# Kernel tuning notes

Measured on AMD Instinct MI355X. Metric: run time of the kernel, lower is better.

Reference implementation:

```python
import jax, jax.numpy as jnp
import numpy as np

KSIZE = 20      # gaussian smoothing kernel size
SIGMA = 2.0     # gaussianSmoothWidth
STRIDE = 4      # strideLen
KLEN = 14       # kernelLen
LN_EPS = 1e-5


def _gauss_smooth(x):
    # x: [B, T, D]; depthwise conv1d along time, padding='same' (torch: left 9, right 10)
    D = x.shape[-1]
    i = jnp.arange(KSIZE, dtype=x.dtype)
    g = jnp.exp(-0.5 * ((i - (KSIZE - 1) / 2.0) / SIGMA) ** 2)
    g = g / jnp.sum(g)
    k = jnp.tile(g[None, None, :], (D, 1, 1))  # [D, 1, KSIZE]
    y = jax.lax.conv_general_dilated(
        jnp.swapaxes(x, 1, 2), k,
        window_strides=(1,), padding=[(9, 10)],
        feature_group_count=D,
        dimension_numbers=('NCW', 'OIW', 'NCW'))
    return jnp.swapaxes(y, 1, 2)


def _qrnn_layer(x, W, b):
    # SpeechBrain QuasiRNNLayer (output_gate=True, unidirectional, zoneout=0)
    # x: [B, T, F]; W: [3H, 2F]; b: [3H]
    xprev = jnp.concatenate([jnp.zeros_like(x[:, :1]), x[:, :-1]], axis=1)
    y = jnp.einsum('btf,gf->btg', jnp.concatenate([x, xprev], axis=-1), W) + b
    z, f, o = jnp.split(y, 3, axis=-1)
    z = jnp.tanh(z)
    f = jax.nn.sigmoid(f)
    fz = f * z
    # recurrence: c_t = f_t*z_t + (1-f_t)*c_{t-1}, c_0-input = 0
    def step(c, ins):
        f_t, fz_t = ins
        c = fz_t + (1.0 - f_t) * c
        return c, c
    c0 = jnp.zeros((f.shape[0], f.shape[2]), f.dtype)
    _, cs = jax.lax.scan(step, c0, (jnp.swapaxes(f, 0, 1), jnp.swapaxes(fz, 0, 1)))
    c = jnp.swapaxes(cs, 0, 1)  # [B, T, H]
    return jax.nn.sigmoid(o) * c


def reference(neuralInput, dayWeights, dayBias, w0, b0, w_rest, b_rest,
              ln_gamma, ln_beta, w_out, b_out, dayIdx):
    x = _gauss_smooth(neuralInput)                    # [B, T, D]
    Wd = dayWeights[dayIdx]                           # [B, D, D]
    bd = dayBias[dayIdx]                              # [B, 1, D]
    x = jnp.einsum('btd,bdk->btk', x, Wd) + bd
    x = x / (1.0 + jnp.abs(x))                        # Softsign
    B, T, D = x.shape
    Tp = (T - KLEN) // STRIDE + 1
    idx = jnp.arange(Tp)[:, None] * STRIDE + jnp.arange(KLEN)[None, :]
    win = x[:, idx, :]                                # [B, Tp, K, D]
    # torch Unfold ordering: channel-major -> feature index = d*KLEN + k
    strided = jnp.transpose(win, (0, 1, 3, 2)).reshape(B, Tp, D * KLEN)
    h = _qrnn_layer(strided, w0, b0)
    for i in range(w_rest.shape[0]):
        h = _qrnn_layer(h, w_rest[i], b_rest[i])
    mu = jnp.mean(h, axis=-1, keepdims=True)
    var = jnp.mean(jnp.square(h - mu), axis=-1, keepdims=True)
    hn = (h - mu) * jax.lax.rsqrt(var + LN_EPS) * ln_gamma + ln_beta
    return jnp.einsum('bth,ch->btc', hn, w_out) + b_out


def setup_inputs() -> dict:
    key = jax.random.key(0)
    ks = jax.random.split(key, 10)
    B, T, D, H, L, NDAYS, C = 32, 2000, 256, 512, 3, 24, 41
    F0 = D * KLEN  # 3584
    inp = {}
    inp['neuralInput'] = jax.random.normal(ks[0], (B, T, D), jnp.float32)
    inp['dayIdx'] = jax.random.randint(ks[1], (B,), 0, NDAYS, jnp.int64 if jax.config.jax_enable_x64 else jnp.int32)
    eye = jnp.eye(D, dtype=jnp.float32)
    inp['dayWeights'] = eye[None] + 0.02 * jax.random.normal(ks[2], (NDAYS, D, D), jnp.float32)
    inp['dayBias'] = jnp.zeros((NDAYS, 1, D), jnp.float32)
    inp['w0'] = jax.random.normal(ks[3], (3 * H, 2 * F0), jnp.float32) / np.sqrt(2 * F0)
    inp['b0'] = jnp.zeros((3 * H,), jnp.float32)
    inp['w_rest'] = jax.random.normal(ks[4], (L - 1, 3 * H, 2 * H), jnp.float32) / np.sqrt(2 * H)
    inp['b_rest'] = jnp.zeros((L - 1, 3 * H), jnp.float32)
    inp['ln_gamma'] = jnp.ones((H,), jnp.float32)
    inp['ln_beta'] = jnp.zeros((H,), jnp.float32)
    inp['w_out'] = jax.random.normal(ks[5], (C, H), jnp.float32) / np.sqrt(H)
    inp['b_out'] = jnp.zeros((C,), jnp.float32)
    return inp
```

## Files before the change

### kernel.cpp

```cpp
#include <hip/hip_runtime.h>
#include <hip/hip_bf16.h>

typedef __hip_bfloat16 bf16;
typedef __attribute__((ext_vector_type(8))) short bf16x8;
typedef __attribute__((ext_vector_type(4))) float f32x4;

#define GT 16
__global__ __launch_bounds__(256) void gauss_kernel(const float* __restrict__ X,
                                                    bf16* __restrict__ Y, int T) {
  int b = blockIdx.y, t0 = blockIdx.x * GT;
  int tid = threadIdx.x;
  __shared__ float xs[GT + 19][256];
  const float* xb = X + (long)b * T * 256;
  for (int r = 0; r < GT + 19; ++r) {
    int tt = t0 + r - 9;
    xs[r][tid] = (tt >= 0 && tt < T) ? xb[(long)tt * 256 + tid] : 0.f;
  }
  __syncthreads();
  float g[20];
  float norm = 0.f;
#pragma unroll
  for (int j = 0; j < 20; ++j) {
    float u = (j - 9.5f) * 0.5f;
    g[j] = expf(-0.5f * u * u);
    norm += g[j];
  }
  float rn = 1.f / norm;
  for (int i = 0; i < GT; ++i) {
    int t = t0 + i;
    if (t >= T) break;
    float acc = 0.f;
#pragma unroll
    for (int j = 0; j < 20; ++j) acc += g[j] * xs[i + j][tid];
    Y[((long)b * T + t) * 256 + tid] = (bf16)(acc * rn);
  }
}

__global__ __launch_bounds__(256) void transpose_day(const float* __restrict__ W,
                                                     bf16* __restrict__ Wt) {
  __shared__ float tile[64][65];
  int d0 = blockIdx.x * 64, g0 = blockIdx.y * 64, day = blockIdx.z;
  const float* Wd = W + (long)day * 65536;
  int tx = threadIdx.x & 63, ty = threadIdx.x >> 6;
  for (int i = 0; i < 16; ++i) {
    int d = ty + i * 4;
    tile[d][tx] = Wd[(long)(d0 + d) * 256 + g0 + tx];
  }
  __syncthreads();
  bf16* out = Wt + (long)day * 65536;
  for (int i = 0; i < 16; ++i) {
    int g = ty + i * 4;
    out[(long)(g0 + g) * 256 + d0 + tx] = (bf16)tile[tx][g];
  }
}

__global__ void buildV_kernel(const float* __restrict__ w0, bf16* __restrict__ V) {
  long idx = (long)blockIdx.x * 256 + threadIdx.x;
  const long total = 18L * 1536 * 256;
  if (idx >= total) return;
  int u = (int)(idx / (1536 * 256));
  int r = (int)(idx % (1536 * 256));
  int g = r >> 8, d = r & 255;
  float v = 0.f;
  if (u < 14) v += w0[(long)g * 7168 + 3584 + d * 14 + u];
  if (u >= 4) v += w0[(long)g * 7168 + d * 14 + (u - 4)];
  V[idx] = (bf16)v;
}

__global__ void conv_wrest(const float* __restrict__ in, bf16* __restrict__ out, long n) {
  long i = (long)blockIdx.x * 256 + threadIdx.x;
  if (i >= n) return;
  long g = i >> 10;
  int k = (int)(i & 1023);
  out[i] = (bf16)in[(g << 10) | (long)(k ^ 512)];
}

__global__ void conv_w0half(const float* __restrict__ in, bf16* __restrict__ out) {
  long i = (long)blockIdx.x * 256 + threadIdx.x;
  const long n = 1536L * 3584;
  if (i >= n) return;
  long g = i / 3584;
  int j = (int)(i - g * 3584);
  out[i] = (bf16)in[g * 7168 + j];
}

__global__ void zero_pads(bf16* __restrict__ h1s, bf16* __restrict__ h2s) {
  int i = blockIdx.x * 256 + threadIdx.x;
  if (i >= 16384) return;
  int b = i >> 9, k = i & 511;
  h1s[(long)b * 498 * 512 + k] = (bf16)0.f;
  h2s[(long)b * 498 * 512 + k] = (bf16)0.f;
}

__global__ __launch_bounds__(256) void mfma_gemm(
    const bf16* __restrict__ A, const bf16* __restrict__ W,
    const float* __restrict__ bias, float* __restrict__ Yf,
    bf16* __restrict__ Yb, const int* __restrict__ dayIdx,
    long astride, int Ta, int D, int rstride, int Tm, int N, int tstride,
    int ntaps, int tap_off0, long wsg, long wst, long dayWStride,
    int dayBStride, int epilogue) {
  int b = blockIdx.z;
  int t0 = blockIdx.y * 128, g0 = blockIdx.x * 128;
  const bf16* Ab = A + (long)b * astride;
  long wbase = 0;
  int boff = 0;
  if (dayIdx) {
    int di = dayIdx[b];
    wbase = (long)di * dayWStride;
    boff = di * dayBStride;
  }
  __shared__ __align__(16) bf16 Al[2][128 * 64];
  __shared__ __align__(16) bf16 Wl[2][128 * 64];
  int tid = threadIdx.x;
  int lane = tid & 63;
  int wave = tid >> 6;
  int wm = (wave >> 1) * 64, wn = (wave & 1) * 64;
  int lr = lane & 15, lg = lane >> 4;
  int srow = tid >> 3, su = tid & 7;
  int nch = D >> 6;
  int niter = ntaps * nch;
  f32x4 acc[4][4] = {};
  bf16x8 ra[4], rw[4];

  auto issue = [&](int it) {
    int tap = it / nch;
    int d0 = (it - tap * nch) << 6;
    int off = tap + tap_off0;
    const bf16* Wtap = W + wbase + (long)tap * wst;
#pragma unroll
    for (int i = 0; i < 4; ++i) {
      int m = srow + i * 32;
      int t = t0 + m;
      int time = t * tstride + off;
      bf16x8 v = {};
      if (t < Tm && time >= 0 && time < Ta)
        v = *reinterpret_cast<const bf16x8*>(Ab + (long)time * rstride + d0 + su * 8);
      ra[i] = v;
      rw[i] = *reinterpret_cast<const bf16x8*>(Wtap + (long)(g0 + m) * wsg + d0 + su * 8);
    }
  };
  auto write_lds = [&](int bufi) {
#pragma unroll
    for (int i = 0; i < 4; ++i) {
      int m = srow + i * 32;
      *reinterpret_cast<bf16x8*>(&Al[bufi][m * 64 + ((su ^ (m & 7)) << 3)]) = ra[i];
      *reinterpret_cast<bf16x8*>(&Wl[bufi][m * 64 + ((su ^ (m & 7)) << 3)]) = rw[i];
    }
  };

  issue(0);
  write_lds(0);
  __syncthreads();
  int cur = 0;
  for (int it = 0; it < niter; ++it) {
    if (it + 1 < niter) issue(it + 1);
#pragma unroll
    for (int kc = 0; kc < 2; ++kc) {
      int ub = kc * 4 + lg;
      bf16x8 af[4], bw[4];
#pragma unroll
      for (int f = 0; f < 4; ++f) {
        int m = wm + f * 16 + lr;
        af[f] = *reinterpret_cast<const bf16x8*>(&Al[cur][m * 64 + ((ub ^ (m & 7)) << 3)]);
        int g = wn + f * 16 + lr;
        bw[f] = *reinterpret_cast<const bf16x8*>(&Wl[cur][g * 64 + ((ub ^ (g & 7)) << 3)]);
      }
      __builtin_amdgcn_s_setprio(1);
#pragma unroll
      for (int fm = 0; fm < 4; ++fm)
#pragma unroll
        for (int fn = 0; fn < 4; ++fn)
          acc[fm][fn] = __builtin_amdgcn_mfma_f32_16x16x32_bf16(af[fm], bw[fn],
                                                                acc[fm][fn], 0, 0, 0);
      __builtin_amdgcn_s_setprio(0);
    }
    if (it + 1 < niter) write_lds(cur ^ 1);
    __syncthreads();
    cur ^= 1;
  }
#pragma unroll
  for (int fn = 0; fn < 4; ++fn) {
    int gcol = g0 + wn + fn * 16 + lr;
    float bb = bias[boff + gcol];
#pragma unroll
    for (int fm = 0; fm < 4; ++fm) {
#pragma unroll
      for (int r = 0; r < 4; ++r) {
        int t = t0 + wm + fm * 16 + lg * 4 + r;
        if (t >= Tm) continue;
        float v = acc[fm][fn][r] + bb;
        if (epilogue == 1) {
          v = v / (1.f + fabsf(v));
          Yb[((long)b * Tm + t) * N + gcol] = (bf16)v;
        } else {
          Yf[((long)b * Tm + t) * N + gcol] = v;
        }
      }
    }
  }
}

__global__ void build_A0(const bf16* __restrict__ xs, bf16* __restrict__ A0) {
  int idx = blockIdx.x * 256 + threadIdx.x;
  if (idx >= 32 * 3584) return;
  int b = idx / 3584, j = idx % 3584;
  int d = j / 14, u = j % 14;
  A0[idx] = xs[((long)b * 2000 + u) * 256 + d];
}

__global__ __launch_bounds__(256) void t0_gemm(const bf16* __restrict__ A0,
                                               const bf16* __restrict__ W0b,
                                               float* __restrict__ part) {
  int g0 = blockIdx.x * 128;
  int ks = blockIdx.y;
  int k0 = ks * 512;
  __shared__ __align__(16) bf16 Wl[128 * 64];
  __shared__ __align__(16) bf16 Alds[32 * 64];
  int tid = threadIdx.x;
  int lane = tid & 63, wave = tid >> 6;
  int wn = wave * 32;
  int lr = lane & 15, lg = lane >> 4;
  int srow = tid >> 3, su = tid & 7;
  f32x4 acc[2][2] = {};
  for (int c = 0; c < 8; ++c) {
    int d0 = k0 + c * 64;
#pragma unroll
    for (int i = 0; i < 4; ++i) {
      int m = srow + i * 32;
      *reinterpret_cast<bf16x8*>(&Wl[m * 64 + ((su ^ (m & 7)) << 3)]) =
          *reinterpret_cast<const bf16x8*>(W0b + (long)(g0 + m) * 3584 + d0 + su * 8);
    }
    {
      int m = srow;
      *reinterpret_cast<bf16x8*>(&Alds[m * 64 + ((su ^ (m & 7)) << 3)]) =
          *reinterpret_cast<const bf16x8*>(A0 + (long)m * 3584 + d0 + su * 8);
    }
    __syncthreads();
#pragma unroll
    for (int kc = 0; kc < 2; ++kc) {
      int ub = kc * 4 + lg;
      bf16x8 am[2], bw[2];
#pragma unroll
      for (int f = 0; f < 2; ++f) {
        int m = f * 16 + lr;
        am[f] = *reinterpret_cast<const bf16x8*>(&Alds[m * 64 + ((ub ^ (m & 7)) << 3)]);
        int g = wn + f * 16 + lr;
        bw[f] = *reinterpret_cast<const bf16x8*>(&Wl[g * 64 + ((ub ^ (g & 7)) << 3)]);
      }
#pragma unroll
      for (int fm = 0; fm < 2; ++fm)
#pragma unroll
        for (int fn = 0; fn < 2; ++fn)
          acc[fm][fn] = __builtin_amdgcn_mfma_f32_16x16x32_bf16(am[fm], bw[fn],
                                                                acc[fm][fn], 0, 0, 0);
    }
    __syncthreads();
  }
#pragma unroll
  for (int fn = 0; fn < 2; ++fn) {
    int gcol = g0 + wn + fn * 16 + lr;
#pragma unroll
    for (int fm = 0; fm < 2; ++fm)
#pragma unroll
      for (int r = 0; r < 4; ++r) {
        int brow = fm * 16 + lg * 4 + r;
        part[((long)ks * 32 + brow) * 1536 + gcol] = acc[fm][fn][r];
      }
  }
}

__global__ void t0_reduce(const float* __restrict__ part, const float* __restrict__ b0,
                          float* __restrict__ y, int Tp) {
  int idx = blockIdx.x * 256 + threadIdx.x;
  if (idx >= 32 * 1536) return;
  int b = idx / 1536, g = idx % 1536;
  float s = b0[g];
#pragma unroll
  for (int k = 0; k < 7; ++k) s += part[((long)k * 32 + b) * 1536 + g];
  y[(long)b * Tp * 1536 + g] = s;
}

#define NC 8
#define LC 63
__device__ __forceinline__ float fsig(float x) { return 1.f / (1.f + __expf(-x)); }
__device__ __forceinline__ float ftanh(float x) { return 1.f - 2.f / (1.f + __expf(2.f * x)); }

__global__ __launch_bounds__(256) void scan_pass1(const float* __restrict__ Yv,
                                                  float* __restrict__ Afac,
                                                  float* __restrict__ Bfac, int Tp) {
  int idx = blockIdx.x * 256 + threadIdx.x;
  int ci = idx >> 14;
  int chain = idx & 16383;
  int b = chain >> 9, hh = chain & 511;
  const float* yb = Yv + (long)b * Tp * 1536 + hh;
  int t0 = ci * LC, t1 = min(t0 + LC, Tp);
  float A = 1.f, Bv = 0.f;
  for (int t = t0; t < t1; ++t) {
    const float* p = yb + (long)t * 1536;
    float z = p[0], f = p[512];
    float fs = fsig(f);
    Bv = fs * ftanh(z) + (1.f - fs) * Bv;
    A *= (1.f - fs);
  }
  Afac[idx] = A;
  Bfac[idx] = Bv;
}

__global__ void scan_pass2(const float* __restrict__ Afac, const float* __restrict__ Bfac,
                           float* __restrict__ cst) {
  int chain = blockIdx.x * 256 + threadIdx.x;
  float c = 0.f;
#pragma unroll
  for (int ci = 0; ci < NC; ++ci) {
    cst[ci * 16384 + chain] = c;
    c = Afac[ci * 16384 + chain] * c + Bfac[ci * 16384 + chain];
  }
}

__global__ __launch_bounds__(256) void scan_pass3(const float* __restrict__ Yv,
                                                  const float* __restrict__ cst,
                                                  bf16* __restrict__ H, int Tp) {
  int idx = blockIdx.x * 256 + threadIdx.x;
  int ci = idx >> 14;
  int chain = idx & 16383;
  int b = chain >> 9, hh = chain & 511;
  const float* yb = Yv + (long)b * Tp * 1536 + hh;
  bf16* hb = H + ((long)b * 498 + 1) * 512 + hh;
  int t0 = ci * LC, t1 = min(t0 + LC, Tp);
  float c = cst[ci * 16384 + chain];
  for (int t = t0; t < t1; ++t) {
    const float* p = yb + (long)t * 1536;
    float z = p[0], f = p[512], o = p[1024];
    float fs = fsig(f);
    c = fs * ftanh(z) + (1.f - fs) * c;
    hb[(long)t * 512] = (bf16)(fsig(o) * c);
  }
}

__global__ __launch_bounds__(256) void ln_out_kernel(
    const bf16* __restrict__ Hs, const float* __restrict__ gamma,
    const float* __restrict__ beta, const float* __restrict__ Wo,
    const float* __restrict__ bo, float* __restrict__ Out) {
  long bt = blockIdx.x;
  int b = (int)(bt / 497), t = (int)(bt % 497);
  const bf16* hrow = Hs + ((long)b * 498 + 1 + t) * 512;
  int tid = threadIdx.x;
  float v0 = (float)hrow[tid], v1 = (float)hrow[tid + 256];
  float s = v0 + v1, s2 = v0 * v0 + v1 * v1;
#pragma unroll
  for (int d = 32; d; d >>= 1) {
    s += __shfl_down(s, d);
    s2 += __shfl_down(s2, d);
  }
  __shared__ float rs[4], rs2[4];
  int wid = tid >> 6, lane = tid & 63;
  if (lane == 0) {
    rs[wid] = s;
    rs2[wid] = s2;
  }
  __syncthreads();
  float sum = rs[0] + rs[1] + rs[2] + rs[3];
  float sum2 = rs2[0] + rs2[1] + rs2[2] + rs2[3];
  float mu = sum * (1.f / 512.f);
  float var = sum2 * (1.f / 512.f) - mu * mu;
  float rstd = rsqrtf(var + 1e-5f);
  __shared__ float hl[512];
  hl[tid] = (v0 - mu) * rstd * gamma[tid] + beta[tid];
  hl[tid + 256] = (v1 - mu) * rstd * gamma[tid + 256] + beta[tid + 256];
  __syncthreads();
  const float4* hp = reinterpret_cast<const float4*>(&hl[lane * 8]);
  float4 h0v = hp[0], h1v = hp[1];
  for (int c = wid; c < 41; c += 4) {
    const float4* wp = reinterpret_cast<const float4*>(Wo + (long)c * 512 + lane * 8);
    float4 w0v = wp[0], w1v = wp[1];
    float a = w0v.x * h0v.x + w0v.y * h0v.y + w0v.z * h0v.z + w0v.w * h0v.w +
              w1v.x * h1v.x + w1v.y * h1v.y + w1v.z * h1v.z + w1v.w * h1v.w;
#pragma unroll
    for (int d = 32; d; d >>= 1) a += __shfl_down(a, d);
    if (lane == 0) Out[bt * 41 + c] = a + bo[c];
  }
}

extern "C" void kernel_launch(void* const* d_in, const int* in_sizes, int n_in,
                              void* d_out, int out_size, void* d_ws, size_t ws_size,
                              hipStream_t stream) {
  const float* neuralInput = (const float*)d_in[0];
  const int* dayIdx = (const int*)d_in[1];
  const float* dayWeights = (const float*)d_in[2];
  const float* dayBias = (const float*)d_in[3];
  const float* w0 = (const float*)d_in[4];
  const float* b0 = (const float*)d_in[5];
  const float* w_rest = (const float*)d_in[6];
  const float* b_rest = (const float*)d_in[7];
  const float* ln_gamma = (const float*)d_in[8];
  const float* ln_beta = (const float*)d_in[9];
  const float* w_out = (const float*)d_in[10];
  const float* b_out = (const float*)d_in[11];
  float* out = (float*)d_out;

  const int B = 32, T = 2000, Tp = 497;

  char* p = (char*)d_ws;
  float* y = (float*)p;   p += 97714176;
  bf16* xs0b = (bf16*)p;  p += 32768000;
  bf16* xs = (bf16*)p;    p += 32768000;
  bf16* Vb = (bf16*)p;    p += 14155776;
  bf16* dWb = (bf16*)p;   p += 3145728;
  bf16* wrb = (bf16*)p;   p += 6291456;
  bf16* w0b = (bf16*)p;   p += 11010048;
  bf16* A0 = (bf16*)p;    p += 229376;
  float* part = (float*)p; p += 1376256;
  bf16* h1s = (bf16*)p;   p += 16320512;
  bf16* h2s = (bf16*)p;   p += 16320512;
  float* Afac = (float*)p; p += 524288;
  float* Bfac = (float*)p; p += 524288;
  float* cst = (float*)p;  p += 524288;

  hipLaunchKernelGGL(zero_pads, dim3(64), dim3(256), 0, stream, h1s, h2s);
  hipLaunchKernelGGL(gauss_kernel, dim3((T + GT - 1) / GT, B), dim3(256), 0, stream,
                     neuralInput, xs0b, T);
  hipLaunchKernelGGL(transpose_day, dim3(4, 4, 24), dim3(256), 0, stream, dayWeights, dWb);
  hipLaunchKernelGGL(buildV_kernel, dim3((18L * 1536 * 256 + 255) / 256), dim3(256), 0,
                     stream, w0, Vb);
  hipLaunchKernelGGL(conv_wrest, dim3((2L * 1536 * 1024 + 255) / 256), dim3(256), 0,
                     stream, w_rest, wrb, 2L * 1536 * 1024);
  hipLaunchKernelGGL(conv_w0half, dim3((1536L * 3584 + 255) / 256), dim3(256), 0,
                     stream, w0, w0b);
  hipLaunchKernelGGL(mfma_gemm, dim3(2, 16, B), dim3(256), 0, stream, xs0b, dWb,
                     dayBias, (float*)nullptr, xs, dayIdx, (long)T * 256, T, 256, 256,
                     T, 256, 1, 1, 0, 256L, 0L, 65536L, 256, 1);
  hipLaunchKernelGGL(build_A0, dim3((32 * 3584 + 255) / 256), dim3(256), 0, stream, xs, A0);
  hipLaunchKernelGGL(t0_gemm, dim3(12, 7), dim3(256), 0, stream, A0, w0b, part);
  hipLaunchKernelGGL(mfma_gemm, dim3(12, 4, B), dim3(256), 0, stream, xs, Vb, b0, y,
                     (bf16*)nullptr, (const int*)nullptr, (long)T * 256, T, 256, 256,
                     Tp, 1536, 4, 18, -4, 256L, 1536L * 256, 0L, 0, 0);
  hipLaunchKernelGGL(t0_reduce, dim3((32 * 1536 + 255) / 256), dim3(256), 0, stream,
                     part, b0, y, Tp);
  hipLaunchKernelGGL(scan_pass1, dim3(512), dim3(256), 0, stream, y, Afac, Bfac, Tp);
  hipLaunchKernelGGL(scan_pass2, dim3(64), dim3(256), 0, stream, Afac, Bfac, cst);
  hipLaunchKernelGGL(scan_pass3, dim3(512), dim3(256), 0, stream, y, cst, h1s, Tp);
  for (int i = 0; i < 2; ++i) {
    bf16* hin = (i == 0) ? h1s : h2s;
    bf16* hout = (i == 0) ? h2s : h1s;
    hipLaunchKernelGGL(mfma_gemm, dim3(12, 4, B), dim3(256), 0, stream, hin,
                       wrb + (long)i * 1536 * 1024, b_rest + (long)i * 1536, y,
                       (bf16*)nullptr, (const int*)nullptr, 498L * 512, Tp, 1024, 512,
                       Tp, 1536, 1, 1, 0, 1024L, 0L, 0L, 0, 0);
    hipLaunchKernelGGL(scan_pass1, dim3(512), dim3(256), 0, stream, y, Afac, Bfac, Tp);
    hipLaunchKernelGGL(scan_pass2, dim3(64), dim3(256), 0, stream, Afac, Bfac, cst);
    hipLaunchKernelGGL(scan_pass3, dim3(512), dim3(256), 0, stream, y, cst, hout, Tp);
  }
  hipLaunchKernelGGL(ln_out_kernel, dim3(B * Tp), dim3(256), 0, stream, h1s,
                     ln_gamma, ln_beta, w_out, b_out, out);
}
```

Before: 944.4 us.

## Use direct global-to-LDS loads, blocked weight layouts, bf16 activated gate outputs

Replaces the register-staged double-buffered GEMM with a single-buffered kernel that loads tiles straight into LDS via global_load_lds. Weights are pre-arranged into 64-wide K-blocks so the loads are contiguous, and out-of-range rows read from a zero page. The GEMM epilogue now applies tanh/sigmoid and stores bf16 instead of fp32 pre-activations, halving the traffic the scan kernels read. The weight-prep kernels are merged into one launch. Dropping double buffering may expose load latency.

```diff
diff --git a/kernel.cpp b/kernel.cpp
--- a/kernel.cpp
+++ b/kernel.cpp
@@ -4,6 +4,9 @@
 typedef __hip_bfloat16 bf16;
 typedef __attribute__((ext_vector_type(8))) short bf16x8;
 typedef __attribute__((ext_vector_type(4))) float f32x4;
+
+__device__ __forceinline__ float fsig(float x) { return 1.f / (1.f + __expf(-x)); }
+__device__ __forceinline__ float ftanh(float x) { return 1.f - 2.f / (1.f + __expf(2.f * x)); }
 
 #define GT 16
 __global__ __launch_bounds__(256) void gauss_kernel(const float* __restrict__ X,
@@ -47,154 +50,150 @@
     tile[d][tx] = Wd[(long)(d0 + d) * 256 + g0 + tx];
   }
   __syncthreads();
-  bf16* out = Wt + (long)day * 65536;
+  bf16* outp = Wt + (((long)day * 4 + (d0 >> 6)) * 256 + g0) * 64;
   for (int i = 0; i < 16; ++i) {
     int g = ty + i * 4;
-    out[(long)(g0 + g) * 256 + d0 + tx] = (bf16)tile[tx][g];
-  }
-}
-
-__global__ void buildV_kernel(const float* __restrict__ w0, bf16* __restrict__ V) {
-  long idx = (long)blockIdx.x * 256 + threadIdx.x;
-  const long total = 18L * 1536 * 256;
-  if (idx >= total) return;
-  int u = (int)(idx / (1536 * 256));
-  int r = (int)(idx % (1536 * 256));
-  int g = r >> 8, d = r & 255;
-  float v = 0.f;
-  if (u < 14) v += w0[(long)g * 7168 + 3584 + d * 14 + u];
-  if (u >= 4) v += w0[(long)g * 7168 + d * 14 + (u - 4)];
-  V[idx] = (bf16)v;
-}
-
-__global__ void conv_wrest(const float* __restrict__ in, bf16* __restrict__ out, long n) {
+    outp[(long)g * 64 + tx] = (bf16)tile[tx][g];
+  }
+}
+
+__global__ void prep_misc(const float* __restrict__ w0, const float* __restrict__ w_rest,
+                          bf16* __restrict__ V2, bf16* __restrict__ wrb2,
+                          bf16* __restrict__ w0b, bf16* __restrict__ h1s,
+                          bf16* __restrict__ h2s, bf16* __restrict__ zpage) {
   long i = (long)blockIdx.x * 256 + threadIdx.x;
-  if (i >= n) return;
-  long g = i >> 10;
-  int k = (int)(i & 1023);
-  out[i] = (bf16)in[(g << 10) | (long)(k ^ 512)];
-}
-
-__global__ void conv_w0half(const float* __restrict__ in, bf16* __restrict__ out) {
-  long i = (long)blockIdx.x * 256 + threadIdx.x;
-  const long n = 1536L * 3584;
-  if (i >= n) return;
-  long g = i / 3584;
-  int j = (int)(i - g * 3584);
-  out[i] = (bf16)in[g * 7168 + j];
-}
-
-__global__ void zero_pads(bf16* __restrict__ h1s, bf16* __restrict__ h2s) {
-  int i = blockIdx.x * 256 + threadIdx.x;
-  if (i >= 16384) return;
-  int b = i >> 9, k = i & 511;
-  h1s[(long)b * 498 * 512 + k] = (bf16)0.f;
-  h2s[(long)b * 498 * 512 + k] = (bf16)0.f;
-}
-
-__global__ __launch_bounds__(256) void mfma_gemm(
+  if (i < 7077888L) {
+    int u = (int)(i / (1536 * 256));
+    int r = (int)(i % (1536 * 256));
+    int g = r >> 8, d = r & 255;
+    float v = 0.f;
+    if (u < 14) v += w0[(long)g * 7168 + 3584 + d * 14 + u];
+    if (u >= 4) v += w0[(long)g * 7168 + d * 14 + (u - 4)];
+    V2[(((long)u * 4 + (d >> 6)) * 1536 + g) * 64 + (d & 63)] = (bf16)v;
+    return;
+  }
+  i -= 7077888L;
+  if (i < 3145728L) {
+    int L = (int)(i / (1536 * 1024));
+    int r = (int)(i % (1536 * 1024));
+    int g = r >> 10, k = r & 1023;
+    float v = w_rest[(long)L * 1536 * 1024 + (long)g * 1024 + (k ^ 512)];
+    wrb2[(long)L * 16 * 1536 * 64 + ((long)(k >> 6) * 1536 + g) * 64 + (k & 63)] = (bf16)v;
+    return;
+  }
+  i -= 3145728L;
+  if (i < 5505024L) {
+    long g = i / 3584;
+    int j = (int)(i - g * 3584);
+    w0b[i] = (bf16)w0[g * 7168 + j];
+    return;
+  }
+  i -= 5505024L;
+  if (i < 16384) {
+    int b = (int)(i >> 9), k = (int)(i & 511);
+    h1s[(long)b * 498 * 512 + k] = (bf16)0.f;
+    h2s[(long)b * 498 * 512 + k] = (bf16)0.f;
+    return;
+  }
+  i -= 16384;
+  if (i < 128) zpage[i] = (bf16)0.f;
+}
+
+__global__ __launch_bounds__(256, 4) void mfma97(
     const bf16* __restrict__ A, const bf16* __restrict__ W,
-    const float* __restrict__ bias, float* __restrict__ Yf,
-    bf16* __restrict__ Yb, const int* __restrict__ dayIdx,
-    long astride, int Ta, int D, int rstride, int Tm, int N, int tstride,
-    int ntaps, int tap_off0, long wsg, long wst, long dayWStride,
-    int dayBStride, int epilogue) {
-  int b = blockIdx.z;
-  int t0 = blockIdx.y * 128, g0 = blockIdx.x * 128;
-  const bf16* Ab = A + (long)b * astride;
+    const float* __restrict__ bias, bf16* __restrict__ Y,
+    const int* __restrict__ dayIdx, const bf16* __restrict__ zpage,
+    long astride, int Ta, int rstride, int Tm, int N, int tstride,
+    int ntaps, int nch, int tap_off0, int NW, long dayWStride,
+    int dayBStride, int mode, int nti, int ngi) {
+  __shared__ __align__(16) char smem[32768];
+  const int id = blockIdx.x;
+  const int bi = id / (ngi * nti);
+  const int rem = id - bi * (ngi * nti);
+  const int gi = rem / nti;
+  const int ti = rem - gi * nti;
+  const int g0 = gi * 128, t0 = ti * 128;
+
+  const bf16* Ab = A + (long)bi * astride;
   long wbase = 0;
   int boff = 0;
   if (dayIdx) {
-    int di = dayIdx[b];
+    int di = dayIdx[bi];
     wbase = (long)di * dayWStride;
     boff = di * dayBStride;
   }
-  __shared__ __align__(16) bf16 Al[2][128 * 64];
-  __shared__ __align__(16) bf16 Wl[2][128 * 64];
-  int tid = threadIdx.x;
-  int lane = tid & 63;
-  int wave = tid >> 6;
-  int wm = (wave >> 1) * 64, wn = (wave & 1) * 64;
-  int lr = lane & 15, lg = lane >> 4;
-  int srow = tid >> 3, su = tid & 7;
-  int nch = D >> 6;
-  int niter = ntaps * nch;
+  const int tid = threadIdx.x;
+  const int lane = tid & 63;
+  const int w = tid >> 6;
+  const int wm = (w >> 1) * 64, wn = (w & 1) * 64;
+  const int lr = lane & 15, lg = lane >> 4;
+
   f32x4 acc[4][4] = {};
-  bf16x8 ra[4], rw[4];
-
-  auto issue = [&](int it) {
-    int tap = it / nch;
-    int d0 = (it - tap * nch) << 6;
-    int off = tap + tap_off0;
-    const bf16* Wtap = W + wbase + (long)tap * wst;
-#pragma unroll
-    for (int i = 0; i < 4; ++i) {
-      int m = srow + i * 32;
-      int t = t0 + m;
-      int time = t * tstride + off;
-      bf16x8 v = {};
-      if (t < Tm && time >= 0 && time < Ta)
-        v = *reinterpret_cast<const bf16x8*>(Ab + (long)time * rstride + d0 + su * 8);
-      ra[i] = v;
-      rw[i] = *reinterpret_cast<const bf16x8*>(Wtap + (long)(g0 + m) * wsg + d0 + su * 8);
+
+  for (int tap = 0; tap < ntaps; ++tap) {
+    for (int dblk = 0; dblk < nch; ++dblk) {
+      int d0 = dblk << 6;
+      int s = tap * nch + dblk;
+      const bf16* Wp = W + wbase + ((long)s * NW + g0) * 64;
+#pragma unroll
+      for (int j = 0; j < 8; ++j) {
+        int q = j * 256 + tid;
+        int qw = j * 256 + w * 64;
+        const bf16* src;
+        if (j < 4) {
+          int row = q >> 3;
+          int u = (q & 7) ^ (row & 7);
+          int time = (t0 + row) * tstride + tap + tap_off0;
+          src = (time >= 0 && time < Ta) ? Ab + (long)time * rstride + d0 + u * 8
+                                         : zpage;
+        } else {
+          int row = (q >> 3) - 128;
+          int u = (q & 7) ^ (row & 7);
+          src = Wp + row * 64 + u * 8;
+        }
+        auto lp = (__attribute__((address_space(3))) void*)(smem + qw * 16);
+        __builtin_amdgcn_global_load_lds(
+            (const __attribute__((address_space(1))) void*)src, lp, 16, 0, 0);
+      }
+      __syncthreads();
+#pragma unroll
+      for (int kc = 0; kc < 2; ++kc) {
+        int ub = kc * 4 + lg;
+        bf16x8 af[4], bw[4];
+#pragma unroll
+        for (int f = 0; f < 4; ++f) {
+          int m = wm + f * 16 + lr;
+          af[f] = *reinterpret_cast<const bf16x8*>(smem + m * 128 + ((ub ^ (m & 7)) << 4));
+          int g = wn + f * 16 + lr;
+          bw[f] = *reinterpret_cast<const bf16x8*>(smem + 16384 + g * 128 +
+                                                   ((ub ^ (g & 7)) << 4));
+        }
+#pragma unroll
+        for (int fm = 0; fm < 4; ++fm)
+#pragma unroll
+          for (int fn = 0; fn < 4; ++fn)
+            acc[fm][fn] = __builtin_amdgcn_mfma_f32_16x16x32_bf16(af[fm], bw[fn],
+                                                                  acc[fm][fn], 0, 0, 0);
+      }
+      __syncthreads();
     }
-  };
-  auto write_lds = [&](int bufi) {
-#pragma unroll
-    for (int i = 0; i < 4; ++i) {
-      int m = srow + i * 32;
-      *reinterpret_cast<bf16x8*>(&Al[bufi][m * 64 + ((su ^ (m & 7)) << 3)]) = ra[i];
-      *reinterpret_cast<bf16x8*>(&Wl[bufi][m * 64 + ((su ^ (m & 7)) << 3)]) = rw[i];
-    }
-  };
-
-  issue(0);
-  write_lds(0);
-  __syncthreads();
-  int cur = 0;
-  for (int it = 0; it < niter; ++it) {
-    if (it + 1 < niter) issue(it + 1);
-#pragma unroll
-    for (int kc = 0; kc < 2; ++kc) {
-      int ub = kc * 4 + lg;
-      bf16x8 af[4], bw[4];
-#pragma unroll
-      for (int f = 0; f < 4; ++f) {
-        int m = wm + f * 16 + lr;
-        af[f] = *reinterpret_cast<const bf16x8*>(&Al[cur][m * 64 + ((ub ^ (m & 7)) << 3)]);
-        int g = wn + f * 16 + lr;
-        bw[f] = *reinterpret_cast<const bf16x8*>(&Wl[cur][g * 64 + ((ub ^ (g & 7)) << 3)]);
-      }
-      __builtin_amdgcn_s_setprio(1);
-#pragma unroll
-      for (int fm = 0; fm < 4; ++fm)
-#pragma unroll
-        for (int fn = 0; fn < 4; ++fn)
-          acc[fm][fn] = __builtin_amdgcn_mfma_f32_16x16x32_bf16(af[fm], bw[fn],
-                                                                acc[fm][fn], 0, 0, 0);
-      __builtin_amdgcn_s_setprio(0);
-    }
-    if (it + 1 < niter) write_lds(cur ^ 1);
-    __syncthreads();
-    cur ^= 1;
   }
 #pragma unroll
   for (int fn = 0; fn < 4; ++fn) {
     int gcol = g0 + wn + fn * 16 + lr;
     float bb = bias[boff + gcol];
+    int sect = gcol >> 9;
 #pragma unroll
     for (int fm = 0; fm < 4; ++fm) {
 #pragma unroll
-      for (int r = 0; r < 4; ++r) {
-        int t = t0 + wm + fm * 16 + lg * 4 + r;
+      for (int rr = 0; rr < 4; ++rr) {
+        int t = t0 + wm + fm * 16 + lg * 4 + rr;
         if (t >= Tm) continue;
-        float v = acc[fm][fn][r] + bb;
-        if (epilogue == 1) {
-          v = v / (1.f + fabsf(v));
-          Yb[((long)b * Tm + t) * N + gcol] = (bf16)v;
-        } else {
-          Yf[((long)b * Tm + t) * N + gcol] = v;
-        }
+        float v = acc[fm][fn][rr] + bb;
+        float e;
+        if (mode == 1) e = v / (1.f + fabsf(v));
+        else e = (sect == 0) ? ftanh(v) : fsig(v);
+        Y[((long)bi * Tm + t) * N + gcol] = (bf16)e;
       }
     }
   }
@@ -270,36 +269,33 @@
 }
 
 __global__ void t0_reduce(const float* __restrict__ part, const float* __restrict__ b0,
-                          float* __restrict__ y, int Tp) {
+                          bf16* __restrict__ yact, int Tp) {
   int idx = blockIdx.x * 256 + threadIdx.x;
   if (idx >= 32 * 1536) return;
   int b = idx / 1536, g = idx % 1536;
   float s = b0[g];
 #pragma unroll
   for (int k = 0; k < 7; ++k) s += part[((long)k * 32 + b) * 1536 + g];
-  y[(long)b * Tp * 1536 + g] = s;
+  float e = (g < 512) ? ftanh(s) : fsig(s);
+  yact[(long)b * Tp * 1536 + g] = (bf16)e;
 }
 
 #define NC 8
 #define LC 63
-__device__ __forceinline__ float fsig(float x) { return 1.f / (1.f + __expf(-x)); }
-__device__ __forceinline__ float ftanh(float x) { return 1.f - 2.f / (1.f + __expf(2.f * x)); }
-
-__global__ __launch_bounds__(256) void scan_pass1(const float* __restrict__ Yv,
+__global__ __launch_bounds__(256) void scan_pass1(const bf16* __restrict__ Yv,
                                                   float* __restrict__ Afac,
                                                   float* __restrict__ Bfac, int Tp) {
   int idx = blockIdx.x * 256 + threadIdx.x;
   int ci = idx >> 14;
   int chain = idx & 16383;
   int b = chain >> 9, hh = chain & 511;
-  const float* yb = Yv + (long)b * Tp * 1536 + hh;
+  const bf16* yb = Yv + (long)b * Tp * 1536 + hh;
   int t0 = ci * LC, t1 = min(t0 + LC, Tp);
   float A = 1.f, Bv = 0.f;
   for (int t = t0; t < t1; ++t) {
-    const float* p = yb + (long)t * 1536;
-    float z = p[0], f = p[512];
-    float fs = fsig(f);
-    Bv = fs * ftanh(z) + (1.f - fs) * Bv;
+    const bf16* p = yb + (long)t * 1536;
+    float zt = (float)p[0], fs = (float)p[512];
+    Bv = fs * zt + (1.f - fs) * Bv;
     A *= (1.f - fs);
   }
   Afac[idx] = A;
@@ -317,23 +313,22 @@
   }
 }
 
-__global__ __launch_bounds__(256) void scan_pass3(const float* __restrict__ Yv,
+__global__ __launch_bounds__(256) void scan_pass3(const bf16* __restrict__ Yv,
                                                   const float* __restrict__ cst,
                                                   bf16* __restrict__ H, int Tp) {
   int idx = blockIdx.x * 256 + threadIdx.x;
   int ci = idx >> 14;
   int chain = idx & 16383;
   int b = chain >> 9, hh = chain & 511;
-  const float* yb = Yv + (long)b * Tp * 1536 + hh;
+  const bf16* yb = Yv + (long)b * Tp * 1536 + hh;
   bf16* hb = H + ((long)b * 498 + 1) * 512 + hh;
   int t0 = ci * LC, t1 = min(t0 + LC, Tp);
   float c = cst[ci * 16384 + chain];
   for (int t = t0; t < t1; ++t) {
-    const float* p = yb + (long)t * 1536;
-    float z = p[0], f = p[512], o = p[1024];
-    float fs = fsig(f);
-    c = fs * ftanh(z) + (1.f - fs) * c;
-    hb[(long)t * 512] = (bf16)(fsig(o) * c);
+    const bf16* p = yb + (long)t * 1536;
+    float zt = (float)p[0], fs = (float)p[512], so = (float)p[1024];
+    c = fs * zt + (1.f - fs) * c;
+    hb[(long)t * 512] = (bf16)(so * c);
   }
 }
 
@@ -401,12 +396,12 @@
   const int B = 32, T = 2000, Tp = 497;
 
   char* p = (char*)d_ws;
-  float* y = (float*)p;   p += 97714176;
+  bf16* yact = (bf16*)p;  p += 48857088;
   bf16* xs0b = (bf16*)p;  p += 32768000;
   bf16* xs = (bf16*)p;    p += 32768000;
-  bf16* Vb = (bf16*)p;    p += 14155776;
-  bf16* dWb = (bf16*)p;   p += 3145728;
-  bf16* wrb = (bf16*)p;   p += 6291456;
+  bf16* V2 = (bf16*)p;    p += 14155776;
+  bf16* dWb2 = (bf16*)p;  p += 3145728;
+  bf16* wrb2 = (bf16*)p;  p += 6291456;
   bf16* w0b = (bf16*)p;   p += 11010048;
   bf16* A0 = (bf16*)p;    p += 229376;
   float* part = (float*)p; p += 1376256;
@@ -415,40 +410,36 @@
   float* Afac = (float*)p; p += 524288;
   float* Bfac = (float*)p; p += 524288;
   float* cst = (float*)p;  p += 524288;
-
-  hipLaunchKernelGGL(zero_pads, dim3(64), dim3(256), 0, stream, h1s, h2s);
+  bf16* zpage = (bf16*)p;  p += 256;
+
+  hipLaunchKernelGGL(prep_misc, dim3((15745152L + 255) / 256), dim3(256), 0, stream,
+                     w0, w_rest, V2, wrb2, w0b, h1s, h2s, zpage);
+  hipLaunchKernelGGL(transpose_day, dim3(4, 4, 24), dim3(256), 0, stream, dayWeights, dWb2);
   hipLaunchKernelGGL(gauss_kernel, dim3((T + GT - 1) / GT, B), dim3(256), 0, stream,
                      neuralInput, xs0b, T);
-  hipLaunchKernelGGL(transpose_day, dim3(4, 4, 24), dim3(256), 0, stream, dayWeights, dWb);
-  hipLaunchKernelGGL(buildV_kernel, dim3((18L * 1536 * 256 + 255) / 256), dim3(256), 0,
-                     stream, w0, Vb);
-  hipLaunchKernelGGL(conv_wrest, dim3((2L * 1536 * 1024 + 255) / 256), dim3(256), 0,
-                     stream, w_rest, wrb, 2L * 1536 * 1024);
-  hipLaunchKernelGGL(conv_w0half, dim3((1536L * 3584 + 255) / 256), dim3(256), 0,
-                     stream, w0, w0b);
-  hipLaunchKernelGGL(mfma_gemm, dim3(2, 16, B), dim3(256), 0, stream, xs0b, dWb,
-                     dayBias, (float*)nullptr, xs, dayIdx, (long)T * 256, T, 256, 256,
-                     T, 256, 1, 1, 0, 256L, 0L, 65536L, 256, 1);
+  hipLaunchKernelGGL(mfma97, dim3(1024), dim3(256), 0, stream, xs0b, dWb2, dayBias,
+                     xs, dayIdx, zpage, (long)T * 256, T, 256, T, 256, 1, 1, 4, 0,
+                     256, 65536L, 256, 1, 16, 2);
   hipLaunchKernelGGL(build_A0, dim3((32 * 3584 + 255) / 256), dim3(256), 0, stream, xs, A0);
   hipLaunchKernelGGL(t0_gemm, dim3(12, 7), dim3(256), 0, stream, A0, w0b, part);
-  hipLaunchKernelGGL(mfma_gemm, dim3(12, 4, B), dim3(256), 0, stream, xs, Vb, b0, y,
-                     (bf16*)nullptr, (const int*)nullptr, (long)T * 256, T, 256, 256,
-                     Tp, 1536, 4, 18, -4, 256L, 1536L * 256, 0L, 0, 0);
+  hipLaunchKernelGGL(mfma97, dim3(1536), dim3(256), 0, stream, xs, V2, b0, yact,
+                     (const int*)nullptr, zpage, (long)T * 256, T, 256, Tp, 1536, 4,
+                     18, 4, -4, 1536, 0L, 0, 2, 4, 12);
   hipLaunchKernelGGL(t0_reduce, dim3((32 * 1536 + 255) / 256), dim3(256), 0, stream,
-                     part, b0, y, Tp);
-  hipLaunchKernelGGL(scan_pass1, dim3(512), dim3(256), 0, stream, y, Afac, Bfac, Tp);
+                     part, b0, yact, Tp);
+  hipLaunchKernelGGL(scan_pass1, dim3(512), dim3(256), 0, stream, yact, Afac, Bfac, Tp);
   hipLaunchKernelGGL(scan_pass2, dim3(64), dim3(256), 0, stream, Afac, Bfac, cst);
-  hipLaunchKernelGGL(scan_pass3, dim3(512), dim3(256), 0, stream, y, cst, h1s, Tp);
+  hipLaunchKernelGGL(scan_pass3, dim3(512), dim3(256), 0, stream, yact, cst, h1s, Tp);
   for (int i = 0; i < 2; ++i) {
     bf16* hin = (i == 0) ? h1s : h2s;
     bf16* hout = (i == 0) ? h2s : h1s;
-    hipLaunchKernelGGL(mfma_gemm, dim3(12, 4, B), dim3(256), 0, stream, hin,
-                       wrb + (long)i * 1536 * 1024, b_rest + (long)i * 1536, y,
-                       (bf16*)nullptr, (const int*)nullptr, 498L * 512, Tp, 1024, 512,
-                       Tp, 1536, 1, 1, 0, 1024L, 0L, 0L, 0, 0);
-    hipLaunchKernelGGL(scan_pass1, dim3(512), dim3(256), 0, stream, y, Afac, Bfac, Tp);
+    hipLaunchKernelGGL(mfma97, dim3(1536), dim3(256), 0, stream, hin,
+                       wrb2 + (long)i * 16 * 1536 * 64, b_rest + (long)i * 1536, yact,
+                       (const int*)nullptr, zpage, 498L * 512, Tp, 512, Tp, 1536, 1,
+                       1, 16, 0, 1536, 0L, 0, 2, 4, 12);
+    hipLaunchKernelGGL(scan_pass1, dim3(512), dim3(256), 0, stream, yact, Afac, Bfac, Tp);
     hipLaunchKernelGGL(scan_pass2, dim3(64), dim3(256), 0, stream, Afac, Bfac, cst);
-    hipLaunchKernelGGL(scan_pass3, dim3(512), dim3(256), 0, stream, y, cst, hout, Tp);
+    hipLaunchKernelGGL(scan_pass3, dim3(512), dim3(256), 0, stream, yact, cst, hout, Tp);
   }
   hipLaunchKernelGGL(ln_out_kernel, dim3(B * Tp), dim3(256), 0, stream, h1s,
                      ln_gamma, ln_beta, w_out, b_out, out);
```

After: 816.9 us. 13.5% less time.
